# Performance work log

Measured on AMD Instinct MI355X. Metric: run time of the kernel, lower is better.

## Reference

```python
import jax, jax.numpy as jnp
import numpy as np

E = 576        # embed_dims
HEADS = 18
NPTS = 12
NF = 3         # num_frames
DD = 2 * NF - 1  # depth of value volume (5)
HD = E // HEADS  # head dim (32)


def _grid_init_bias():
    # Faithful reproduction of init_weights() for sampling_offsets.bias
    theta = np.arange(8) * (2.0 * np.pi / 8)
    yaw = np.stack([np.cos(theta), np.sin(theta), np.zeros(8)], -1)
    roll = np.stack([np.zeros(8), np.cos(theta), np.sin(theta)], -1)
    pitch = np.stack([np.cos(theta), np.zeros(8), np.sin(theta)], -1)
    g = np.concatenate([yaw, pitch[[1, 2, 3, 5, 6, 7]], roll[[1, 3, 5, 7]]], 0)  # (18,3)
    g = g / np.abs(g).max(-1, keepdims=True)
    g = np.tile(g[:, None, None, :], (1, 1, NPTS, 1))              # (18,1,12,3)
    g = g * np.arange(1, NPTS + 1, dtype=np.float64)[None, None, :, None]
    return g.reshape(-1).astype(np.float32)                        # (18*12*3,)


def setup_inputs() -> dict:
    key = jax.random.key(0)
    ks = jax.random.split(key, 6)
    bs, h, w = 2, 64, 80
    nq = h * w
    lim = float(np.sqrt(6.0 / (E + E)))  # xavier uniform for square E x E
    return {
        "query": jax.random.normal(ks[0], (bs, nq, E), jnp.float32),
        "value": jax.random.normal(ks[1], (bs, nq * DD, E), jnp.float32),
        "query_pos": jax.random.normal(ks[2], (bs, nq, E), jnp.float32),
        "W_off": jnp.zeros((E, HEADS * NPTS * 3), jnp.float32),  # constant_init 0
        "b_off": jnp.asarray(_grid_init_bias()),
        "W_attn": jnp.zeros((E, HEADS * NPTS), jnp.float32),
        "b_attn": jnp.zeros((HEADS * NPTS,), jnp.float32),
        "W_v": jax.random.uniform(ks[3], (E, E), jnp.float32, -lim, lim),
        "b_v": jnp.zeros((E,), jnp.float32),
        "W_out": jax.random.uniform(ks[4], (E, E), jnp.float32, -lim, lim),
        "b_out": jnp.zeros((E,), jnp.float32),
        "h": 64,
        "w": 80,
    }


def _deform_attn_3d(value, loc, attn, D, H, W):
    # value: (bs, D*H*W, heads, hd)  token order: depth-major (D, H, W)
    # loc:   (bs, nq, heads, np, 3)  normalized (x, y, z) in [0,1]
    # attn:  (bs, nq, heads, np)
    bs, _, heads, hd = value.shape
    nq = loc.shape[1]
    # (bs, heads, D*H*W, hd) flat spatial for gathers
    v = value.reshape(bs, D, H, W, heads, hd).transpose(0, 4, 1, 2, 3, 5)
    v = v.reshape(bs, heads, D * H * W, hd)
    lt = jnp.moveaxis(loc, 2, 1)    # (bs, heads, nq, np, 3)
    at = jnp.moveaxis(attn, 2, 1)   # (bs, heads, nq, np)
    # grid_sample(align_corners=False) coordinate convention: pix = u*size - 0.5
    x = lt[..., 0] * W - 0.5
    y = lt[..., 1] * H - 0.5
    z = lt[..., 2] * D - 0.5
    x0 = jnp.floor(x); y0 = jnp.floor(y); z0 = jnp.floor(z)
    fx = x - x0; fy = y - y0; fz = z - z0
    acc = jnp.zeros((bs, heads, nq, NPTS, hd), v.dtype)
    for dz in (0, 1):
        for dy in (0, 1):
            for dx in (0, 1):
                xi = x0 + dx; yi = y0 + dy; zi = z0 + dz
                wgt = ((fx if dx else 1.0 - fx)
                       * (fy if dy else 1.0 - fy)
                       * (fz if dz else 1.0 - fz))
                valid = ((xi >= 0) & (xi < W) & (yi >= 0) & (yi < H)
                         & (zi >= 0) & (zi < D))
                xc = jnp.clip(xi, 0, W - 1).astype(jnp.int32)
                yc = jnp.clip(yi, 0, H - 1).astype(jnp.int32)
                zc = jnp.clip(zi, 0, D - 1).astype(jnp.int32)
                idx = ((zc * H + yc) * W + xc).reshape(bs, heads, nq * NPTS)
                g = jnp.take_along_axis(v, idx[..., None], axis=2)
                g = g.reshape(bs, heads, nq, NPTS, hd)
                acc = acc + g * (wgt * valid.astype(v.dtype))[..., None]
    out = jnp.einsum("bhqp,bhqpd->bhqd", at, acc)  # softmax-weighted sum over points
    return out.transpose(0, 2, 1, 3).reshape(bs, nq, heads * hd)


def _forward(query, value, query_pos, W_off, b_off, W_attn, b_attn,
             W_v, b_v, W_out, b_out, h, w):
    bs, nq, _ = query.shape
    q = query + query_pos
    v = (value @ W_v + b_v).reshape(bs, nq * DD, HEADS, HD)
    offs = (q @ W_off + b_off).reshape(bs, nq, HEADS, NPTS, 3)
    attn = jax.nn.softmax((q @ W_attn + b_attn).reshape(bs, nq, HEADS, NPTS), axis=-1)
    # reference points: pixel centers normalized, z = 0
    ry, rx = jnp.meshgrid((jnp.arange(h, dtype=jnp.float32) + 0.5) / h,
                          (jnp.arange(w, dtype=jnp.float32) + 0.5) / w,
                          indexing="ij")
    ref = jnp.stack([rx.reshape(-1), ry.reshape(-1),
                     jnp.zeros(h * w, jnp.float32)], -1)  # (nq, 3)
    norm = jnp.array([w, h, NF], jnp.float32)  # NOTE: z normalized by num_frames (as in source)
    loc = ref[None, :, None, None, :] + offs / norm
    out = _deform_attn_3d(v, loc, attn, DD, h, w)
    return out @ W_out + b_out  # dropout is identity at eval


def reference(query, value, query_pos, W_off, b_off, W_attn, b_attn,
              W_v, b_v, W_out, b_out, h, w):
    return _forward(query, value, query_pos, W_off, b_off, W_attn, b_attn,
                    W_v, b_v, W_out, b_out, h, w)
```

## Files before the change

kernel.cpp:

```cpp
#include <hip/hip_runtime.h>
#include <cstdint>

#define E_DIM   576
#define HEADS   18
#define NPTS    12
#define DDEPTH  5
#define HDIM    32
#define BSZ     2
#define GH      64
#define GW      80
#define NQ      (GH*GW)
#define NTOK    (NQ*DDEPTH)
#define MIXW    864
#define BQ_TOT  (BSZ*NQ)

typedef __attribute__((ext_vector_type(8))) short short8;
typedef __attribute__((ext_vector_type(4))) float f32x4;

__device__ __forceinline__ float b2f_lo(uint32_t u) {
    union { uint32_t u; float f; } v; v.u = u << 16; return v.f;
}
__device__ __forceinline__ float b2f_hi(uint32_t u) {
    union { uint32_t u; float f; } v; v.u = u & 0xffff0000u; return v.f;
}
__device__ __forceinline__ ushort f2b(float f) {
    union { float f; uint32_t u; } v; v.f = f;
    return (ushort)((v.u + 0x7fffu + ((v.u >> 16) & 1u)) >> 16);
}

__global__ void cast_kernel(const float* __restrict__ in, ushort* __restrict__ out, int n4) {
    int i = blockIdx.x * blockDim.x + threadIdx.x;
    if (i >= n4) return;
    const float4 v = reinterpret_cast<const float4*>(in)[i];
    ushort4 o; o.x = f2b(v.x); o.y = f2b(v.y); o.z = f2b(v.z); o.w = f2b(v.w);
    reinterpret_cast<ushort4*>(out)[i] = o;
}

__global__ void cast_add_kernel(const float* __restrict__ a, const float* __restrict__ b,
                                ushort* __restrict__ out, int n4) {
    int i = blockIdx.x * blockDim.x + threadIdx.x;
    if (i >= n4) return;
    const float4 va = reinterpret_cast<const float4*>(a)[i];
    const float4 vb = reinterpret_cast<const float4*>(b)[i];
    ushort4 o;
    o.x = f2b(va.x + vb.x); o.y = f2b(va.y + vb.y);
    o.z = f2b(va.z + vb.z); o.w = f2b(va.w + vb.w);
    reinterpret_cast<ushort4*>(out)[i] = o;
}

__global__ void prep_weights(const float* __restrict__ W_v, const float* __restrict__ W_out,
                             const float* __restrict__ W_off, const float* __restrict__ W_attn,
                             const float* __restrict__ b_off, const float* __restrict__ b_attn,
                             ushort* __restrict__ wt_v, ushort* __restrict__ wt_out,
                             ushort* __restrict__ wt_mix, float* __restrict__ bias_mix) {
    int idx = blockIdx.x * blockDim.x + threadIdx.x;
    if (idx < 864) bias_mix[idx] = (idx < 648) ? b_off[idx] : b_attn[idx - 648];
    if (idx < 331776) {
        int n = idx / E_DIM, k = idx - n * E_DIM;
        wt_v[idx] = f2b(W_v[(size_t)k * E_DIM + n]);
    } else if (idx < 663552) {
        int j = idx - 331776;
        int n = j / E_DIM, k = j - n * E_DIM;
        wt_out[j] = f2b(W_out[(size_t)k * E_DIM + n]);
    } else if (idx < 1161216) {
        int j = idx - 663552;
        int n = j / E_DIM, k = j - n * E_DIM;
        float v = (n < 648) ? W_off[(size_t)k * 648 + n] : W_attn[(size_t)k * 216 + (n - 648)];
        wt_mix[j] = f2b(v);
    }
}

#define TM 128
#define TN 96
#define BK 32

__device__ __forceinline__ void async_cp16(const ushort* gsrc, ushort* ldst) {
    __builtin_amdgcn_global_load_lds(
        (const __attribute__((address_space(1))) void*)gsrc,
        (__attribute__((address_space(3))) void*)ldst, 16, 0, 0);
}

template <typename OutT>
__global__ void gemm_mfma(const ushort* __restrict__ A, const ushort* __restrict__ Bt,
                          const float* __restrict__ bias, OutT* __restrict__ C,
                          int M, int N, int K, int ldc) {
    __shared__ __align__(16) ushort Asb[TM * BK];
    __shared__ __align__(16) ushort Bsb[TN * BK];
    const int tid  = threadIdx.x;
    const int wave = tid >> 6;
    const int lane = tid & 63;
    const int m16  = lane & 15;
    const int quad = lane >> 4;
    const int row0 = blockIdx.x * TM;
    const int n0   = blockIdx.y * TN;

    const f32x4 zero = {0.f, 0.f, 0.f, 0.f};
    f32x4 acc[2][6];
    #pragma unroll
    for (int rt = 0; rt < 2; ++rt)
        #pragma unroll
        for (int ct = 0; ct < 6; ++ct) acc[rt][ct] = zero;

    const int srow = lane >> 2;
    const int scol = (lane & 3) * 8;

    for (int k0 = 0; k0 < K; k0 += BK) {
        #pragma unroll
        for (int c = 0; c < 2; ++c) {
            const int ch = wave + c * 4;
            async_cp16(A + (size_t)(row0 + ch * 16 + srow) * K + k0 + scol,
                       Asb + ch * 512 + lane * 8);
        }
        {
            const int ch = wave;
            if (ch < 6)
                async_cp16(Bt + (size_t)(n0 + ch * 16 + srow) * K + k0 + scol,
                           Bsb + ch * 512 + lane * 8);
            const int ch2 = wave + 4;
            if (ch2 < 6)
                async_cp16(Bt + (size_t)(n0 + ch2 * 16 + srow) * K + k0 + scol,
                           Bsb + ch2 * 512 + lane * 8);
        }
        __syncthreads();

        short8 afrag[2], bfrag[6];
        #pragma unroll
        for (int rt = 0; rt < 2; ++rt)
            afrag[rt] = *reinterpret_cast<const short8*>(
                Asb + (wave * 32 + rt * 16 + m16) * BK + quad * 8);
        #pragma unroll
        for (int ct = 0; ct < 6; ++ct)
            bfrag[ct] = *reinterpret_cast<const short8*>(
                Bsb + (ct * 16 + m16) * BK + quad * 8);

        #pragma unroll
        for (int rt = 0; rt < 2; ++rt)
            #pragma unroll
            for (int ct = 0; ct < 6; ++ct)
                acc[rt][ct] = __builtin_amdgcn_mfma_f32_16x16x32_bf16(
                    afrag[rt], bfrag[ct], acc[rt][ct], 0, 0, 0);

        __syncthreads();
    }

    #pragma unroll
    for (int ct = 0; ct < 6; ++ct) {
        const int col = n0 + ct * 16 + m16;
        const float bcol = bias[col];
        #pragma unroll
        for (int rt = 0; rt < 2; ++rt) {
            #pragma unroll
            for (int r = 0; r < 4; ++r) {
                const int row = row0 + wave * 32 + rt * 16 + quad * 4 + r;
                const float val = acc[rt][ct][r] + bcol;
                if constexpr (__is_same(OutT, float)) {
                    C[(size_t)row * ldc + col] = val;
                } else {
                    C[(size_t)row * ldc + col] = f2b(val);
                }
            }
        }
    }
}

__global__ void __launch_bounds__(256, 8)
deform_kernel(const ushort* __restrict__ vbuf,
              const float* __restrict__ mix,
              ushort* __restrict__ aout) {
    const int gl   = threadIdx.x >> 4;
    const int l    = threadIdx.x & 15;
    const int head = blockIdx.x / 640;
    const int bq   = (blockIdx.x % 640) * 16 + gl;
    const int q    = bq % NQ;
    const int b    = bq / NQ;
    const int qx   = q % GW;
    const int qy   = q / GW;

    const float* mrow = mix + (size_t)bq * MIXW;

    float lg = (l < NPTS) ? mrow[648 + head * NPTS + l] : -1e30f;
    float mx = lg;
    #pragma unroll
    for (int mk = 1; mk < 16; mk <<= 1) mx = fmaxf(mx, __shfl_xor(mx, mk, 16));
    float e = (l < NPTS) ? __expf(lg - mx) : 0.f;
    float s = e;
    #pragma unroll
    for (int mk = 1; mk < 16; mk <<= 1) s += __shfl_xor(s, mk, 16);

    float    cw[8];
    uint32_t coff[8];
    uint32_t mask = 0;
    {
        const float ap = e / s;
        const int pl = (l < NPTS) ? l : 0;
        const int ob = (head * NPTS + pl) * 3;
        const float ox = mrow[ob + 0];
        const float oy = mrow[ob + 1];
        const float oz = mrow[ob + 2];
        const float x = (float)qx + ox;
        const float y = (float)qy + oy;
        const float z = oz * (5.0f / 3.0f) - 0.5f;
        const float x0f = floorf(x), y0f = floorf(y), z0f = floorf(z);
        const int x0 = (int)x0f, y0 = (int)y0f, z0 = (int)z0f;
        const float fx = x - x0f, fy = y - y0f, fz = z - z0f;

        #pragma unroll
        for (int dz = 0; dz < 2; ++dz) {
            const int zi = z0 + dz;
            const bool zv = (zi >= 0) & (zi < DDEPTH);
            const int zc = min(max(zi, 0), DDEPTH - 1);
            const float wz = dz ? fz : 1.f - fz;
            #pragma unroll
            for (int dy = 0; dy < 2; ++dy) {
                const int yi = y0 + dy;
                const bool yv = (yi >= 0) & (yi < GH);
                const int yc = min(max(yi, 0), GH - 1);
                const float wy = dy ? fy : 1.f - fy;
                #pragma unroll
                for (int dx = 0; dx < 2; ++dx) {
                    const int xi = x0 + dx;
                    const bool xv = (xi >= 0) & (xi < GW);
                    const int xc = min(max(xi, 0), GW - 1);
                    const float wx = dx ? fx : 1.f - fx;
                    const int i = dz * 4 + dy * 2 + dx;
                    const bool valid = zv & yv & xv & (l < NPTS);
                    cw[i]   = ap * wz * wy * wx;
                    coff[i] = (uint32_t)((zc * GH + yc) * GW + xc) * (E_DIM / 2);
                    mask |= (valid ? (1u << i) : 0u);
                }
            }
        }
    }

    const uint32_t* vb = reinterpret_cast<const uint32_t*>(vbuf)
                         + (size_t)b * NTOK * (E_DIM / 2) + head * (HDIM / 2) + l;
    float o0 = 0.f, o1 = 0.f;
    #pragma unroll
    for (int p = 0; p < NPTS; ++p) {
        const uint32_t msk = (uint32_t)__shfl((int)mask, p, 16);
        if (msk == 0) continue;
        #pragma unroll
        for (int i = 0; i < 8; ++i) {
            if (msk & (1u << i)) {
                const float    w   = __shfl(cw[i], p, 16);
                const uint32_t off = (uint32_t)__shfl((int)coff[i], p, 16);
                const uint32_t pair = vb[off];
                o0 += w * b2f_lo(pair);
                o1 += w * b2f_hi(pair);
            }
        }
    }
    const uint32_t packed = (uint32_t)f2b(o0) | ((uint32_t)f2b(o1) << 16);
    reinterpret_cast<uint32_t*>(aout)[(size_t)bq * (E_DIM / 2) + head * (HDIM / 2) + l] = packed;
}

extern "C" void kernel_launch(void* const* d_in, const int* in_sizes, int n_in,
                              void* d_out, int out_size, void* d_ws, size_t ws_size,
                              hipStream_t stream) {
    const float* query     = (const float*)d_in[0];
    const float* value     = (const float*)d_in[1];
    const float* query_pos = (const float*)d_in[2];
    const float* W_off     = (const float*)d_in[3];
    const float* b_off     = (const float*)d_in[4];
    const float* W_attn    = (const float*)d_in[5];
    const float* b_attn    = (const float*)d_in[6];
    const float* W_v       = (const float*)d_in[7];
    const float* b_v       = (const float*)d_in[8];
    const float* W_out     = (const float*)d_in[9];
    const float* b_out     = (const float*)d_in[10];
    float* out = (float*)d_out;

    char* ws = (char*)d_ws;
    ushort* vbuf     = (ushort*)(ws);
    ushort* val_bf16 = (ushort*)(ws + 58982400);
    ushort* aout     = val_bf16;
    ushort* q_bf16   = (ushort*)(ws + 117964800);
    float*  mixb     = (float*) (ws + 129761280);
    ushort* wt_v     = (ushort*)(ws + 165150720);
    ushort* wt_out   = (ushort*)(ws + 165814272);
    ushort* wt_mix   = (ushort*)(ws + 166477824);
    float*  bias_mix = (float*) (ws + 167473152);

    cast_kernel<<<(51200 * 576 / 4 + 255) / 256, 256, 0, stream>>>(value, val_bf16, 51200 * 576 / 4);
    cast_add_kernel<<<(10240 * 576 / 4 + 255) / 256, 256, 0, stream>>>(query, query_pos, q_bf16, 10240 * 576 / 4);
    prep_weights<<<(1161216 + 255) / 256, 256, 0, stream>>>(
        W_v, W_out, W_off, W_attn, b_off, b_attn, wt_v, wt_out, wt_mix, bias_mix);

    gemm_mfma<float><<<dim3(10240 / TM, MIXW / TN), 256, 0, stream>>>(
        q_bf16, wt_mix, bias_mix, mixb, BSZ * NQ, MIXW, E_DIM, MIXW);

    gemm_mfma<ushort><<<dim3(51200 / TM, E_DIM / TN), 256, 0, stream>>>(
        val_bf16, wt_v, b_v, vbuf, BSZ * NTOK, E_DIM, E_DIM, E_DIM);

    deform_kernel<<<HEADS * 640, 256, 0, stream>>>(vbuf, mixb, aout);

    gemm_mfma<float><<<dim3(10240 / TM, E_DIM / TN), 256, 0, stream>>>(
        aout, wt_out, b_out, out, BSZ * NQ, E_DIM, E_DIM, E_DIM);
}
```

Measured before the change: 395.5 us.

## Fuse fp32-to-bf16 casts into GEMM A-loads and swizzle LDS tiles

Removes the separate cast and cast-add kernels. The GEMMs now read fp32 value, or query plus query_pos, directly, convert to bf16 in registers and store into LDS. This avoids writing and re-reading bf16 copies of large activations. It also adds an XOR swizzle to the LDS layout to reduce bank conflicts on fragment reads. In exchange, A-tile loads become synchronous register loads instead of async global-to-LDS copies, and each GEMM reads twice the bytes in fp32.

```diff
diff --git a/kernel.cpp b/kernel.cpp
--- a/kernel.cpp
+++ b/kernel.cpp
@@ -12,7 +12,6 @@
 #define NQ      (GH*GW)
 #define NTOK    (NQ*DDEPTH)
 #define MIXW    864
-#define BQ_TOT  (BSZ*NQ)
 
 typedef __attribute__((ext_vector_type(8))) short short8;
 typedef __attribute__((ext_vector_type(4))) float f32x4;
@@ -27,25 +26,11 @@
     union { float f; uint32_t u; } v; v.f = f;
     return (ushort)((v.u + 0x7fffu + ((v.u >> 16) & 1u)) >> 16);
 }
-
-__global__ void cast_kernel(const float* __restrict__ in, ushort* __restrict__ out, int n4) {
-    int i = blockIdx.x * blockDim.x + threadIdx.x;
-    if (i >= n4) return;
-    const float4 v = reinterpret_cast<const float4*>(in)[i];
-    ushort4 o; o.x = f2b(v.x); o.y = f2b(v.y); o.z = f2b(v.z); o.w = f2b(v.w);
-    reinterpret_cast<ushort4*>(out)[i] = o;
-}
-
-__global__ void cast_add_kernel(const float* __restrict__ a, const float* __restrict__ b,
-                                ushort* __restrict__ out, int n4) {
-    int i = blockIdx.x * blockDim.x + threadIdx.x;
-    if (i >= n4) return;
-    const float4 va = reinterpret_cast<const float4*>(a)[i];
-    const float4 vb = reinterpret_cast<const float4*>(b)[i];
-    ushort4 o;
-    o.x = f2b(va.x + vb.x); o.y = f2b(va.y + vb.y);
-    o.z = f2b(va.z + vb.z); o.w = f2b(va.w + vb.w);
-    reinterpret_cast<ushort4*>(out)[i] = o;
+__device__ __forceinline__ uint32_t pkbf(float a, float b) {
+    uint32_t ua = __float_as_uint(a), ub = __float_as_uint(b);
+    ua = ua + 0x7fffu + ((ua >> 16) & 1u);
+    ub = ub + 0x7fffu + ((ub >> 16) & 1u);
+    return (ua >> 16) | (ub & 0xffff0000u);
 }
 
 __global__ void prep_weights(const float* __restrict__ W_v, const float* __restrict__ W_out,
@@ -80,10 +65,23 @@
         (__attribute__((address_space(3))) void*)ldst, 16, 0, 0);
 }
 
-template <typename OutT>
-__global__ void gemm_mfma(const ushort* __restrict__ A, const ushort* __restrict__ Bt,
-                          const float* __restrict__ bias, OutT* __restrict__ C,
-                          int M, int N, int K, int ldc) {
+__device__ __forceinline__ void dec_swz(int P, int& row, int& kc) {
+    const int t = P >> 3;
+    const int u = (P & 7) ^ (t & 7);
+    row = (t << 1) | (u >> 2);
+    kc  = u & 3;
+}
+__device__ __forceinline__ int swz_off(int row, int kc) {
+    const int t = row >> 1;
+    const int u = ((row & 1) << 2) | kc;
+    return t * 64 + ((u ^ (t & 7)) << 3);
+}
+
+template <int AMODE, typename OutT>
+__global__ __launch_bounds__(256) void
+gemm_mfma(const void* __restrict__ Ap, const float* __restrict__ A2,
+          const ushort* __restrict__ Bt, const float* __restrict__ bias,
+          OutT* __restrict__ C, int M, int N, int K, int ldc) {
     __shared__ __align__(16) ushort Asb[TM * BK];
     __shared__ __align__(16) ushort Bsb[TN * BK];
     const int tid  = threadIdx.x;
@@ -101,37 +99,87 @@
         #pragma unroll
         for (int ct = 0; ct < 6; ++ct) acc[rt][ct] = zero;
 
-    const int srow = lane >> 2;
-    const int scol = (lane & 3) * 8;
+    int bn0, bkc0, bn1, bkc1;
+    dec_swz(wave * 64 + lane, bn0, bkc0);
+    dec_swz((wave + 4) * 64 + lane, bn1, bkc1);
+    const ushort* gB0 = Bt + (size_t)(n0 + bn0) * K + bkc0 * 8;
+    const ushort* gB1 = Bt + (size_t)(n0 + bn1) * K + bkc1 * 8;
+    ushort* dB0 = Bsb + wave * 512;
+    ushort* dB1 = Bsb + (wave + 4) * 512;
+
+    const ushort* gA0 = nullptr; const ushort* gA1 = nullptr;
+    ushort* dA0 = nullptr; ushort* dA1 = nullptr;
+    const float* fA0 = nullptr; const float* fA1 = nullptr;
+    const float* fB0a = nullptr; const float* fB1a = nullptr;
+    uint32_t* wA0 = nullptr; uint32_t* wA1 = nullptr;
+    if constexpr (AMODE == 0) {
+        const ushort* A = (const ushort*)Ap;
+        int m, kc;
+        dec_swz(wave * 64 + lane, m, kc);
+        gA0 = A + (size_t)(row0 + m) * K + kc * 8;
+        dA0 = Asb + wave * 512;
+        dec_swz((wave + 4) * 64 + lane, m, kc);
+        gA1 = A + (size_t)(row0 + m) * K + kc * 8;
+        dA1 = Asb + (wave + 4) * 512;
+    } else {
+        const float* A = (const float*)Ap;
+        int m, kc;
+        dec_swz(tid, m, kc);
+        fA0 = A + (size_t)(row0 + m) * K + kc * 8;
+        if constexpr (AMODE == 2) fB0a = A2 + (size_t)(row0 + m) * K + kc * 8;
+        wA0 = (uint32_t*)(Asb + tid * 8);
+        dec_swz(tid + 256, m, kc);
+        fA1 = A + (size_t)(row0 + m) * K + kc * 8;
+        if constexpr (AMODE == 2) fB1a = A2 + (size_t)(row0 + m) * K + kc * 8;
+        wA1 = (uint32_t*)(Asb + (tid + 256) * 8);
+    }
+
+    int aoff[2], boff[6];
+    #pragma unroll
+    for (int rt = 0; rt < 2; ++rt)
+        aoff[rt] = swz_off(wave * 32 + rt * 16 + m16, quad);
+    #pragma unroll
+    for (int ct = 0; ct < 6; ++ct)
+        boff[ct] = swz_off(ct * 16 + m16, quad);
 
     for (int k0 = 0; k0 < K; k0 += BK) {
-        #pragma unroll
-        for (int c = 0; c < 2; ++c) {
-            const int ch = wave + c * 4;
-            async_cp16(A + (size_t)(row0 + ch * 16 + srow) * K + k0 + scol,
-                       Asb + ch * 512 + lane * 8);
-        }
-        {
-            const int ch = wave;
-            if (ch < 6)
-                async_cp16(Bt + (size_t)(n0 + ch * 16 + srow) * K + k0 + scol,
-                           Bsb + ch * 512 + lane * 8);
-            const int ch2 = wave + 4;
-            if (ch2 < 6)
-                async_cp16(Bt + (size_t)(n0 + ch2 * 16 + srow) * K + k0 + scol,
-                           Bsb + ch2 * 512 + lane * 8);
+        async_cp16(gB0 + k0, dB0);
+        if (wave < 2) async_cp16(gB1 + k0, dB1);
+        if constexpr (AMODE == 0) {
+            async_cp16(gA0 + k0, dA0);
+            async_cp16(gA1 + k0, dA1);
+        } else {
+            float4 x0 = *reinterpret_cast<const float4*>(fA0 + k0);
+            float4 x1 = *reinterpret_cast<const float4*>(fA0 + k0 + 4);
+            float4 y0 = *reinterpret_cast<const float4*>(fA1 + k0);
+            float4 y1 = *reinterpret_cast<const float4*>(fA1 + k0 + 4);
+            if constexpr (AMODE == 2) {
+                const float4 p0 = *reinterpret_cast<const float4*>(fB0a + k0);
+                const float4 p1 = *reinterpret_cast<const float4*>(fB0a + k0 + 4);
+                const float4 q0 = *reinterpret_cast<const float4*>(fB1a + k0);
+                const float4 q1 = *reinterpret_cast<const float4*>(fB1a + k0 + 4);
+                x0.x += p0.x; x0.y += p0.y; x0.z += p0.z; x0.w += p0.w;
+                x1.x += p1.x; x1.y += p1.y; x1.z += p1.z; x1.w += p1.w;
+                y0.x += q0.x; y0.y += q0.y; y0.z += q0.z; y0.w += q0.w;
+                y1.x += q1.x; y1.y += q1.y; y1.z += q1.z; y1.w += q1.w;
+            }
+            uint4 o;
+            o.x = pkbf(x0.x, x0.y); o.y = pkbf(x0.z, x0.w);
+            o.z = pkbf(x1.x, x1.y); o.w = pkbf(x1.z, x1.w);
+            *reinterpret_cast<uint4*>(wA0) = o;
+            o.x = pkbf(y0.x, y0.y); o.y = pkbf(y0.z, y0.w);
+            o.z = pkbf(y1.x, y1.y); o.w = pkbf(y1.z, y1.w);
+            *reinterpret_cast<uint4*>(wA1) = o;
         }
         __syncthreads();
 
         short8 afrag[2], bfrag[6];
         #pragma unroll
         for (int rt = 0; rt < 2; ++rt)
-            afrag[rt] = *reinterpret_cast<const short8*>(
-                Asb + (wave * 32 + rt * 16 + m16) * BK + quad * 8);
+            afrag[rt] = *reinterpret_cast<const short8*>(Asb + aoff[rt]);
         #pragma unroll
         for (int ct = 0; ct < 6; ++ct)
-            bfrag[ct] = *reinterpret_cast<const short8*>(
-                Bsb + (ct * 16 + m16) * BK + quad * 8);
+            bfrag[ct] = *reinterpret_cast<const short8*>(Bsb + boff[ct]);
 
         #pragma unroll
         for (int rt = 0; rt < 2; ++rt)
@@ -272,28 +320,24 @@
 
     char* ws = (char*)d_ws;
     ushort* vbuf     = (ushort*)(ws);
-    ushort* val_bf16 = (ushort*)(ws + 58982400);
-    ushort* aout     = val_bf16;
-    ushort* q_bf16   = (ushort*)(ws + 117964800);
-    float*  mixb     = (float*) (ws + 129761280);
-    ushort* wt_v     = (ushort*)(ws + 165150720);
-    ushort* wt_out   = (ushort*)(ws + 165814272);
-    ushort* wt_mix   = (ushort*)(ws + 166477824);
-    float*  bias_mix = (float*) (ws + 167473152);
-
-    cast_kernel<<<(51200 * 576 / 4 + 255) / 256, 256, 0, stream>>>(value, val_bf16, 51200 * 576 / 4);
-    cast_add_kernel<<<(10240 * 576 / 4 + 255) / 256, 256, 0, stream>>>(query, query_pos, q_bf16, 10240 * 576 / 4);
+    ushort* aout     = (ushort*)(ws + 58982400);
+    float*  mixb     = (float*) (ws + 70778880);
+    ushort* wt_v     = (ushort*)(ws + 106168320);
+    ushort* wt_out   = (ushort*)(ws + 106831872);
+    ushort* wt_mix   = (ushort*)(ws + 107495424);
+    float*  bias_mix = (float*) (ws + 108490752);
+
     prep_weights<<<(1161216 + 255) / 256, 256, 0, stream>>>(
         W_v, W_out, W_off, W_attn, b_off, b_attn, wt_v, wt_out, wt_mix, bias_mix);
 
-    gemm_mfma<float><<<dim3(10240 / TM, MIXW / TN), 256, 0, stream>>>(
-        q_bf16, wt_mix, bias_mix, mixb, BSZ * NQ, MIXW, E_DIM, MIXW);
-
-    gemm_mfma<ushort><<<dim3(51200 / TM, E_DIM / TN), 256, 0, stream>>>(
-        val_bf16, wt_v, b_v, vbuf, BSZ * NTOK, E_DIM, E_DIM, E_DIM);
+    gemm_mfma<2, float><<<dim3(10240 / TM, MIXW / TN), 256, 0, stream>>>(
+        query, query_pos, wt_mix, bias_mix, mixb, BSZ * NQ, MIXW, E_DIM, MIXW);
+
+    gemm_mfma<1, ushort><<<dim3(51200 / TM, E_DIM / TN), 256, 0, stream>>>(
+        value, nullptr, wt_v, b_v, vbuf, BSZ * NTOK, E_DIM, E_DIM, E_DIM);
 
     deform_kernel<<<HEADS * 640, 256, 0, stream>>>(vbuf, mixb, aout);
 
-    gemm_mfma<float><<<dim3(10240 / TM, E_DIM / TN), 256, 0, stream>>>(
-        aout, wt_out, b_out, out, BSZ * NQ, E_DIM, E_DIM, E_DIM);
-}
+    gemm_mfma<0, float><<<dim3(10240 / TM, E_DIM / TN), 256, 0, stream>>>(
+        aout, nullptr, wt_out, b_out, out, BSZ * NQ, E_DIM, E_DIM, E_DIM);
+}
```

Result: slower. 415.6 us (+5.1%).

## Fuse value fp32-to-bf16 cast into value-projection GEMM and swizzle LDS layout

Applied to the files above, without the earlier changes.

Replaces the separate value cast kernel plus generic GEMM with a dedicated gemm_value kernel that loads fp32 value rows, converts them to bf16 into LDS, and computes the full 576-wide output per 32-row block. This removes a full bf16 round trip of the large value tensor through global memory. The generic GEMM also gets an XOR-swizzled LDS layout to reduce bank conflicts, and the casts use packed bf16 stores. The new value kernel keeps a large LDS footprint (A tile plus a 576x32 B tile), which may limit occupancy, and it re-streams all of W_v for every 32-row block.

```diff
diff --git a/kernel.cpp b/kernel.cpp
--- a/kernel.cpp
+++ b/kernel.cpp
@@ -12,7 +12,6 @@
 #define NQ      (GH*GW)
 #define NTOK    (NQ*DDEPTH)
 #define MIXW    864
-#define BQ_TOT  (BSZ*NQ)
 
 typedef __attribute__((ext_vector_type(8))) short short8;
 typedef __attribute__((ext_vector_type(4))) float f32x4;
@@ -27,13 +26,29 @@
     union { float f; uint32_t u; } v; v.f = f;
     return (ushort)((v.u + 0x7fffu + ((v.u >> 16) & 1u)) >> 16);
 }
-
-__global__ void cast_kernel(const float* __restrict__ in, ushort* __restrict__ out, int n4) {
-    int i = blockIdx.x * blockDim.x + threadIdx.x;
-    if (i >= n4) return;
-    const float4 v = reinterpret_cast<const float4*>(in)[i];
-    ushort4 o; o.x = f2b(v.x); o.y = f2b(v.y); o.z = f2b(v.z); o.w = f2b(v.w);
-    reinterpret_cast<ushort4*>(out)[i] = o;
+__device__ __forceinline__ uint32_t pkbf(float a, float b) {
+    uint32_t ua = __float_as_uint(a), ub = __float_as_uint(b);
+    ua = ua + 0x7fffu + ((ua >> 16) & 1u);
+    ub = ub + 0x7fffu + ((ub >> 16) & 1u);
+    return (ua >> 16) | (ub & 0xffff0000u);
+}
+
+__device__ __forceinline__ void async_cp16(const ushort* gsrc, ushort* ldst) {
+    __builtin_amdgcn_global_load_lds(
+        (const __attribute__((address_space(1))) void*)gsrc,
+        (__attribute__((address_space(3))) void*)ldst, 16, 0, 0);
+}
+
+__device__ __forceinline__ void dec_swz(int P, int& row, int& kc) {
+    const int t = P >> 3;
+    const int u = (P & 7) ^ (t & 7);
+    row = (t << 1) | (u >> 2);
+    kc  = u & 3;
+}
+__device__ __forceinline__ int swz_off(int row, int kc) {
+    const int t = row >> 1;
+    const int u = ((row & 1) << 2) | kc;
+    return t * 64 + ((u ^ (t & 7)) << 3);
 }
 
 __global__ void cast_add_kernel(const float* __restrict__ a, const float* __restrict__ b,
@@ -42,10 +57,10 @@
     if (i >= n4) return;
     const float4 va = reinterpret_cast<const float4*>(a)[i];
     const float4 vb = reinterpret_cast<const float4*>(b)[i];
-    ushort4 o;
-    o.x = f2b(va.x + vb.x); o.y = f2b(va.y + vb.y);
-    o.z = f2b(va.z + vb.z); o.w = f2b(va.w + vb.w);
-    reinterpret_cast<ushort4*>(out)[i] = o;
+    uint2 o;
+    o.x = pkbf(va.x + vb.x, va.y + vb.y);
+    o.y = pkbf(va.z + vb.z, va.w + vb.w);
+    reinterpret_cast<uint2*>(out)[i] = o;
 }
 
 __global__ void prep_weights(const float* __restrict__ W_v, const float* __restrict__ W_out,
@@ -74,16 +89,11 @@
 #define TN 96
 #define BK 32
 
-__device__ __forceinline__ void async_cp16(const ushort* gsrc, ushort* ldst) {
-    __builtin_amdgcn_global_load_lds(
-        (const __attribute__((address_space(1))) void*)gsrc,
-        (__attribute__((address_space(3))) void*)ldst, 16, 0, 0);
-}
-
 template <typename OutT>
-__global__ void gemm_mfma(const ushort* __restrict__ A, const ushort* __restrict__ Bt,
-                          const float* __restrict__ bias, OutT* __restrict__ C,
-                          int M, int N, int K, int ldc) {
+__global__ __launch_bounds__(256) void
+gemm_mfma(const ushort* __restrict__ A, const ushort* __restrict__ Bt,
+          const float* __restrict__ bias, OutT* __restrict__ C,
+          int M, int N, int K, int ldc) {
     __shared__ __align__(16) ushort Asb[TM * BK];
     __shared__ __align__(16) ushort Bsb[TN * BK];
     const int tid  = threadIdx.x;
@@ -101,37 +111,43 @@
         #pragma unroll
         for (int ct = 0; ct < 6; ++ct) acc[rt][ct] = zero;
 
-    const int srow = lane >> 2;
-    const int scol = (lane & 3) * 8;
+    int r, kc;
+    dec_swz(wave * 64 + lane, r, kc);
+    const ushort* gA0 = A + (size_t)(row0 + r) * K + kc * 8;
+    dec_swz((wave + 4) * 64 + lane, r, kc);
+    const ushort* gA1 = A + (size_t)(row0 + r) * K + kc * 8;
+    ushort* dA0 = Asb + (wave * 64 + lane) * 8;
+    ushort* dA1 = Asb + ((wave + 4) * 64 + lane) * 8;
+
+    dec_swz(wave * 64 + lane, r, kc);
+    const ushort* gB0 = Bt + (size_t)(n0 + r) * K + kc * 8;
+    dec_swz((wave + 4) * 64 + lane, r, kc);
+    const ushort* gB1 = Bt + (size_t)(n0 + r) * K + kc * 8;
+    ushort* dB0 = Bsb + (wave * 64 + lane) * 8;
+    ushort* dB1 = Bsb + ((wave + 4) * 64 + lane) * 8;
+
+    int aoff[2], boff[6];
+    #pragma unroll
+    for (int rt = 0; rt < 2; ++rt)
+        aoff[rt] = swz_off(wave * 32 + rt * 16 + m16, quad);
+    #pragma unroll
+    for (int ct = 0; ct < 6; ++ct)
+        boff[ct] = swz_off(ct * 16 + m16, quad);
 
     for (int k0 = 0; k0 < K; k0 += BK) {
-        #pragma unroll
-        for (int c = 0; c < 2; ++c) {
-            const int ch = wave + c * 4;
-            async_cp16(A + (size_t)(row0 + ch * 16 + srow) * K + k0 + scol,
-                       Asb + ch * 512 + lane * 8);
-        }
-        {
-            const int ch = wave;
-            if (ch < 6)
-                async_cp16(Bt + (size_t)(n0 + ch * 16 + srow) * K + k0 + scol,
-                           Bsb + ch * 512 + lane * 8);
-            const int ch2 = wave + 4;
-            if (ch2 < 6)
-                async_cp16(Bt + (size_t)(n0 + ch2 * 16 + srow) * K + k0 + scol,
-                           Bsb + ch2 * 512 + lane * 8);
-        }
+        async_cp16(gA0 + k0, dA0);
+        async_cp16(gA1 + k0, dA1);
+        async_cp16(gB0 + k0, dB0);
+        if (wave < 2) async_cp16(gB1 + k0, dB1);
         __syncthreads();
 
         short8 afrag[2], bfrag[6];
         #pragma unroll
         for (int rt = 0; rt < 2; ++rt)
-            afrag[rt] = *reinterpret_cast<const short8*>(
-                Asb + (wave * 32 + rt * 16 + m16) * BK + quad * 8);
+            afrag[rt] = *reinterpret_cast<const short8*>(Asb + aoff[rt]);
         #pragma unroll
         for (int ct = 0; ct < 6; ++ct)
-            bfrag[ct] = *reinterpret_cast<const short8*>(
-                Bsb + (ct * 16 + m16) * BK + quad * 8);
+            bfrag[ct] = *reinterpret_cast<const short8*>(Bsb + boff[ct]);
 
         #pragma unroll
         for (int rt = 0; rt < 2; ++rt)
@@ -150,14 +166,105 @@
         #pragma unroll
         for (int rt = 0; rt < 2; ++rt) {
             #pragma unroll
-            for (int r = 0; r < 4; ++r) {
-                const int row = row0 + wave * 32 + rt * 16 + quad * 4 + r;
-                const float val = acc[rt][ct][r] + bcol;
+            for (int rr = 0; rr < 4; ++rr) {
+                const int row = row0 + wave * 32 + rt * 16 + quad * 4 + rr;
+                const float val = acc[rt][ct][rr] + bcol;
                 if constexpr (__is_same(OutT, float)) {
                     C[(size_t)row * ldc + col] = val;
                 } else {
                     C[(size_t)row * ldc + col] = f2b(val);
                 }
+            }
+        }
+    }
+}
+
+#define VTM 32
+
+__global__ __launch_bounds__(256) void
+gemm_value(const float* __restrict__ A, const ushort* __restrict__ Bt,
+           const float* __restrict__ bias, ushort* __restrict__ C) {
+    __shared__ __align__(16) ushort Asb[VTM * E_DIM];
+    __shared__ __align__(16) ushort Bsb[E_DIM * BK];
+    const int tid  = threadIdx.x;
+    const int wave = tid >> 6;
+    const int lane = tid & 63;
+    const int m16  = lane & 15;
+    const int quad = lane >> 4;
+    const int row0 = blockIdx.x * VTM;
+
+    #pragma unroll
+    for (int i = 0; i < 9; ++i) {
+        const int ch = tid + i * 256;
+        const int rr = ch / 72, cc = ch - rr * 72;
+        const float* src = A + (size_t)(row0 + rr) * E_DIM + cc * 8;
+        const float4 x0 = *reinterpret_cast<const float4*>(src);
+        const float4 x1 = *reinterpret_cast<const float4*>(src + 4);
+        uint4 o;
+        o.x = pkbf(x0.x, x0.y); o.y = pkbf(x0.z, x0.w);
+        o.z = pkbf(x1.x, x1.y); o.w = pkbf(x1.z, x1.w);
+        *reinterpret_cast<uint4*>(Asb + (rr * 72 + (cc ^ (rr & 7))) * 8) = o;
+    }
+
+    int bsoff[9];
+    #pragma unroll
+    for (int i = 0; i < 9; ++i) {
+        int n, kc;
+        dec_swz(i * 256 + tid, n, kc);
+        bsoff[i] = n * E_DIM + kc * 8;
+    }
+    ushort* const bdst = Bsb + tid * 8;
+
+    const f32x4 zero = {0.f, 0.f, 0.f, 0.f};
+    f32x4 acc[2][9];
+    #pragma unroll
+    for (int rt = 0; rt < 2; ++rt)
+        #pragma unroll
+        for (int ct = 0; ct < 9; ++ct) acc[rt][ct] = zero;
+
+    int boff[9];
+    #pragma unroll
+    for (int ct = 0; ct < 9; ++ct)
+        boff[ct] = swz_off(wave * 144 + ct * 16 + m16, quad);
+    const int ar0 = (m16) * 72;
+    const int ar1 = (m16 + 16) * 72;
+    const int ax0 = m16 & 7;
+    const int ax1 = (m16 + 16) & 7;
+
+    for (int kt = 0; kt < E_DIM / BK; ++kt) {
+        #pragma unroll
+        for (int i = 0; i < 9; ++i)
+            async_cp16(Bt + bsoff[i] + kt * BK, bdst + i * 2048);
+        __syncthreads();
+
+        const int c = kt * 4 + quad;
+        short8 afrag[2], bfrag[9];
+        afrag[0] = *reinterpret_cast<const short8*>(Asb + (ar0 + (c ^ ax0)) * 8);
+        afrag[1] = *reinterpret_cast<const short8*>(Asb + (ar1 + (c ^ ax1)) * 8);
+        #pragma unroll
+        for (int ct = 0; ct < 9; ++ct)
+            bfrag[ct] = *reinterpret_cast<const short8*>(Bsb + boff[ct]);
+
+        #pragma unroll
+        for (int rt = 0; rt < 2; ++rt)
+            #pragma unroll
+            for (int ct = 0; ct < 9; ++ct)
+                acc[rt][ct] = __builtin_amdgcn_mfma_f32_16x16x32_bf16(
+                    afrag[rt], bfrag[ct], acc[rt][ct], 0, 0, 0);
+
+        __syncthreads();
+    }
+
+    #pragma unroll
+    for (int ct = 0; ct < 9; ++ct) {
+        const int col = wave * 144 + ct * 16 + m16;
+        const float bcol = bias[col];
+        #pragma unroll
+        for (int rt = 0; rt < 2; ++rt) {
+            #pragma unroll
+            for (int rr = 0; rr < 4; ++rr) {
+                const int row = row0 + rt * 16 + quad * 4 + rr;
+                C[(size_t)row * E_DIM + col] = f2b(acc[rt][ct][rr] + bcol);
             }
         }
     }
@@ -272,26 +379,25 @@
 
     char* ws = (char*)d_ws;
     ushort* vbuf     = (ushort*)(ws);
-    ushort* val_bf16 = (ushort*)(ws + 58982400);
-    ushort* aout     = val_bf16;
-    ushort* q_bf16   = (ushort*)(ws + 117964800);
-    float*  mixb     = (float*) (ws + 129761280);
-    ushort* wt_v     = (ushort*)(ws + 165150720);
-    ushort* wt_out   = (ushort*)(ws + 165814272);
-    ushort* wt_mix   = (ushort*)(ws + 166477824);
-    float*  bias_mix = (float*) (ws + 167473152);
-
-    cast_kernel<<<(51200 * 576 / 4 + 255) / 256, 256, 0, stream>>>(value, val_bf16, 51200 * 576 / 4);
-    cast_add_kernel<<<(10240 * 576 / 4 + 255) / 256, 256, 0, stream>>>(query, query_pos, q_bf16, 10240 * 576 / 4);
+    ushort* aout     = (ushort*)(ws + 58982400);
+    ushort* q_bf16   = (ushort*)(ws + 70778880);
+    float*  mixb     = (float*) (ws + 82575360);
+    ushort* wt_v     = (ushort*)(ws + 117964800);
+    ushort* wt_out   = (ushort*)(ws + 118628352);
+    ushort* wt_mix   = (ushort*)(ws + 119291904);
+    float*  bias_mix = (float*) (ws + 120287232);
+
     prep_weights<<<(1161216 + 255) / 256, 256, 0, stream>>>(
         W_v, W_out, W_off, W_attn, b_off, b_attn, wt_v, wt_out, wt_mix, bias_mix);
 
+    cast_add_kernel<<<(10240 * 576 / 4 + 255) / 256, 256, 0, stream>>>(
+        query, query_pos, q_bf16, 10240 * 576 / 4);
+
+    gemm_value<<<51200 / VTM, 256, 0, stream>>>(value, wt_v, b_v, vbuf);
+
     gemm_mfma<float><<<dim3(10240 / TM, MIXW / TN), 256, 0, stream>>>(
         q_bf16, wt_mix, bias_mix, mixb, BSZ * NQ, MIXW, E_DIM, MIXW);
 
-    gemm_mfma<ushort><<<dim3(51200 / TM, E_DIM / TN), 256, 0, stream>>>(
-        val_bf16, wt_v, b_v, vbuf, BSZ * NTOK, E_DIM, E_DIM, E_DIM);
-
     deform_kernel<<<HEADS * 640, 256, 0, stream>>>(vbuf, mixb, aout);
 
     gemm_mfma<float><<<dim3(10240 / TM, E_DIM / TN), 256, 0, stream>>>(
```

New measurement: 414.9 us. 1.05x slower.
